# Kernel tuning notes

Measured on AMD Instinct MI355X. Metric: run time of the kernel, lower is better.

The kernel has to match this reference:

```python
import jax, jax.numpy as jnp
import numpy as np

B, S, H, E, A = 64, 1024, 1024, 1024, 1024

def setup_inputs() -> dict:
    key = jax.random.key(0)
    k1, k2, k3, k4, k5 = jax.random.split(key, 5)
    return {
        "decoder_state": jax.random.normal(k1, (B, H), dtype=jnp.float32),
        "encoder_outputs": jax.random.normal(k2, (B, S, E), dtype=jnp.float32),
        "src_mask": jnp.ones((B, S), dtype=bool),
        "W_a": jax.random.normal(k3, (H, A), dtype=jnp.float32) / np.sqrt(H),
        "U_a": jax.random.normal(k4, (E, A), dtype=jnp.float32) / np.sqrt(E),
        "v_a": jax.random.normal(k5, (A,), dtype=jnp.float32) / np.sqrt(A),
    }

def reference(decoder_state, encoder_outputs, src_mask, W_a, U_a, v_a):
    # k_dec: [B, 1, A], k_enc: [B, S, A]
    k_dec = jnp.einsum('bh,ha->ba', decoder_state, W_a)[:, None, :]
    k_enc = jnp.einsum('bse,ea->bsa', encoder_outputs, U_a)
    att_hidden = jnp.tanh(k_dec + k_enc)
    scores = jnp.einsum('bsa,a->bs', att_hidden, v_a)
    scores = scores + (~src_mask).astype(scores.dtype) * (-1e9)
    weights = jax.nn.softmax(scores, axis=-1)
    ctx = jnp.einsum('bs,bse->be', weights, encoder_outputs)
    return (ctx, weights)
```

## Files before the change

kernel.cpp:

```cpp
#include <hip/hip_runtime.h>
#include <hip/hip_bf16.h>
#include <math.h>

#define NB 64
#define NS 1024
#define NH 1024
#define NE 1024
#define NA 1024

#define BM 128
#define BN 128
#define BK 64

typedef __attribute__((ext_vector_type(8))) short bf16x8;
typedef __attribute__((ext_vector_type(4))) float f32x4;

__device__ __forceinline__ unsigned short f2bf(float x) {
    __hip_bfloat16 h = __float2bfloat16(x);
    return *reinterpret_cast<unsigned short*>(&h);
}
__device__ __forceinline__ float bf2f(unsigned short u) {
    __hip_bfloat16 h = *reinterpret_cast<__hip_bfloat16*>(&u);
    return __bfloat162float(h);
}
__device__ __forceinline__ float tanh_fast(float x) {
    float ax = fabsf(x);
    float e = __expf(-2.f * ax);
    float r = (1.f - e) / (1.f + e);
    return x < 0.f ? -r : r;
}
__device__ __forceinline__ int swz(int row, int colBf16) {
    return (row * 128 + colBf16 * 2) ^ ((row & 7) << 4);
}

__global__ __launch_bounds__(256) void split_uat_kernel(
    const float* __restrict__ Ua,
    unsigned short* __restrict__ uatHi, unsigned short* __restrict__ uatLo)
{
    __shared__ float tile[32][33];
    const int e0 = blockIdx.x * 32, a0 = blockIdx.y * 32;
    const int tx = threadIdx.x & 31, ty = threadIdx.x >> 5;
#pragma unroll
    for (int j = 0; j < 4; ++j)
        tile[ty + j * 8][tx] = Ua[(size_t)(e0 + ty + j * 8) * NA + a0 + tx];
    __syncthreads();
#pragma unroll
    for (int j = 0; j < 4; ++j) {
        const int a = a0 + ty + j * 8;
        const float x = tile[tx][ty + j * 8];
        const unsigned short h = f2bf(x);
        const unsigned short l = f2bf(x - bf2f(h));
        uatHi[(size_t)a * NE + e0 + tx] = h;
        uatLo[(size_t)a * NE + e0 + tx] = l;
    }
}

__global__ __launch_bounds__(256) void kdec_kernel(
    const float* __restrict__ dec, const float* __restrict__ Wa,
    float* __restrict__ kdec)
{
    __shared__ float dls[NH];
    const int b = blockIdx.x;
    const int a = blockIdx.y * 256 + threadIdx.x;
    for (int i = threadIdx.x; i < NH; i += 256) dls[i] = dec[b * NH + i];
    __syncthreads();
    float acc = 0.f;
#pragma unroll 8
    for (int h = 0; h < NH; ++h) acc += dls[h] * Wa[(size_t)h * NA + a];
    kdec[b * NA + a] = acc;
}

__global__ __launch_bounds__(256, 2) void scores_kernel(
    const float* __restrict__ enc,
    const unsigned short* __restrict__ uatHi, const unsigned short* __restrict__ uatLo,
    const float* __restrict__ kdec, const float* __restrict__ va,
    float* __restrict__ scores)
{
    __shared__ __align__(16) char aHi[BM * BK * 2];
    __shared__ __align__(16) char aLo[BM * BK * 2];
    __shared__ __align__(16) char bHi[BN * BK * 2];
    __shared__ __align__(16) char bLo[BN * BK * 2];
    __shared__ float scLds[2][BM];

    const int t    = threadIdx.x;
    const int b    = blockIdx.y;
    const int s0   = blockIdx.x * BM;
    const int lane = t & 63;
    const int wid  = t >> 6;
    const int wr   = wid >> 1;
    const int wc   = wid & 1;
    const int lr   = lane & 15;
    const int lk   = (lane >> 4) * 8;

    const float* encB = enc + ((size_t)b * NS + s0) * NE;

    float scp[4][4];
#pragma unroll
    for (int i = 0; i < 4; ++i)
#pragma unroll
        for (int r = 0; r < 4; ++r) scp[i][r] = 0.f;

    for (int ac = 0; ac < NA / BN; ++ac) {
        const int a0 = ac * BN;
        f32x4 acc[4][4];
#pragma unroll
        for (int fi = 0; fi < 4; ++fi)
#pragma unroll
            for (int fj = 0; fj < 4; ++fj) acc[fi][fj] = (f32x4){0.f, 0.f, 0.f, 0.f};

        for (int e0 = 0; e0 < NE; e0 += BK) {
            __syncthreads();
#pragma unroll
            for (int it = 0; it < 8; ++it) {
                const int flat = t + it * 256;
                const int row  = flat >> 4;
                const int c4   = (flat & 15) * 4;
                const float4 v = *reinterpret_cast<const float4*>(
                    encB + (size_t)row * NE + e0 + c4);
                ushort4 h, l;
                h.x = f2bf(v.x); l.x = f2bf(v.x - bf2f(h.x));
                h.y = f2bf(v.y); l.y = f2bf(v.y - bf2f(h.y));
                h.z = f2bf(v.z); l.z = f2bf(v.z - bf2f(h.z));
                h.w = f2bf(v.w); l.w = f2bf(v.w - bf2f(h.w));
                *reinterpret_cast<ushort4*>(aHi + swz(row, c4)) = h;
                *reinterpret_cast<ushort4*>(aLo + swz(row, c4)) = l;
            }
#pragma unroll
            for (int it = 0; it < 4; ++it) {
                const int flat = t + it * 256;
                const int row  = flat >> 3;
                const int c8   = (flat & 7) * 8;
                const size_t g = (size_t)(a0 + row) * NE + e0 + c8;
                *reinterpret_cast<int4*>(bHi + swz(row, c8)) =
                    *reinterpret_cast<const int4*>(uatHi + g);
                *reinterpret_cast<int4*>(bLo + swz(row, c8)) =
                    *reinterpret_cast<const int4*>(uatLo + g);
            }
            __syncthreads();

#pragma unroll
            for (int ks = 0; ks < BK; ks += 32) {
                bf16x8 aH[4], aL[4], bH[4], bL[4];
#pragma unroll
                for (int f = 0; f < 4; ++f) {
                    aH[f] = *reinterpret_cast<const bf16x8*>(aHi + swz(wr * 64 + f * 16 + lr, ks + lk));
                    aL[f] = *reinterpret_cast<const bf16x8*>(aLo + swz(wr * 64 + f * 16 + lr, ks + lk));
                    bH[f] = *reinterpret_cast<const bf16x8*>(bHi + swz(wc * 64 + f * 16 + lr, ks + lk));
                    bL[f] = *reinterpret_cast<const bf16x8*>(bLo + swz(wc * 64 + f * 16 + lr, ks + lk));
                }
#pragma unroll
                for (int fi = 0; fi < 4; ++fi)
#pragma unroll
                    for (int fj = 0; fj < 4; ++fj) {
                        acc[fi][fj] = __builtin_amdgcn_mfma_f32_16x16x32_bf16(aH[fi], bH[fj], acc[fi][fj], 0, 0, 0);
                        acc[fi][fj] = __builtin_amdgcn_mfma_f32_16x16x32_bf16(aH[fi], bL[fj], acc[fi][fj], 0, 0, 0);
                        acc[fi][fj] = __builtin_amdgcn_mfma_f32_16x16x32_bf16(aL[fi], bH[fj], acc[fi][fj], 0, 0, 0);
                    }
            }
        }

#pragma unroll
        for (int fj = 0; fj < 4; ++fj) {
            const int a = a0 + wc * 64 + fj * 16 + lr;
            const float kd = kdec[(size_t)b * NA + a];
            const float vv = va[a];
#pragma unroll
            for (int fi = 0; fi < 4; ++fi)
#pragma unroll
                for (int r = 0; r < 4; ++r)
                    scp[fi][r] += tanh_fast(kd + acc[fi][fj][r]) * vv;
        }
    }

#pragma unroll
    for (int fi = 0; fi < 4; ++fi)
#pragma unroll
        for (int r = 0; r < 4; ++r) {
            float v = scp[fi][r];
            v += __shfl_xor(v, 1);
            v += __shfl_xor(v, 2);
            v += __shfl_xor(v, 4);
            v += __shfl_xor(v, 8);
            if (lr == 0)
                scLds[wc][wr * 64 + fi * 16 + (lane >> 4) * 4 + r] = v;
        }
    __syncthreads();
    if (t < BM)
        scores[(size_t)b * NS + s0 + t] = scLds[0][t] + scLds[1][t];
}

__global__ __launch_bounds__(256) void softmax_kernel(
    const float* __restrict__ scores, const int* __restrict__ mask,
    float* __restrict__ out )
{
    __shared__ float red[8];
    const int b = blockIdx.x;
    const int t = threadIdx.x;
    float v[4];
    float mx = -INFINITY;
#pragma unroll
    for (int i = 0; i < 4; ++i) {
        const int s = t + i * 256;
        float x = scores[b * NS + s];
        if (mask[b * NS + s] == 0) x += -1e9f;
        v[i] = x;
        mx = fmaxf(mx, x);
    }
    for (int off = 1; off < 64; off <<= 1) mx = fmaxf(mx, __shfl_xor(mx, off));
    const int wid = t >> 6;
    if ((t & 63) == 0) red[wid] = mx;
    __syncthreads();
    mx = fmaxf(fmaxf(red[0], red[1]), fmaxf(red[2], red[3]));
    float sum = 0.f;
#pragma unroll
    for (int i = 0; i < 4; ++i) { v[i] = expf(v[i] - mx); sum += v[i]; }
    for (int off = 1; off < 64; off <<= 1) sum += __shfl_xor(sum, off);
    if ((t & 63) == 0) red[4 + wid] = sum;
    __syncthreads();
    sum = red[4] + red[5] + red[6] + red[7];
    const float inv = 1.f / sum;
#pragma unroll
    for (int i = 0; i < 4; ++i) {
        const int s = t + i * 256;
        out[NB * NE + b * NS + s] = v[i] * inv;
        out[b * NE + s] = 0.f;
    }
}

__global__ __launch_bounds__(256) void ctx_kernel(
    const float* __restrict__ enc, const float* __restrict__ w,
    float* __restrict__ ctx)
{
    __shared__ float wls[128];
    const int b  = blockIdx.x;
    const int ec = blockIdx.y;
    const int ss = blockIdx.z;
    const int t  = threadIdx.x;
    if (t < 128) wls[t] = w[b * NS + ss * 128 + t];
    __syncthreads();
    const int e = ec * 256 + t;
    const float* p = enc + ((size_t)b * NS + ss * 128) * NE + e;
    float acc = 0.f;
#pragma unroll 4
    for (int s = 0; s < 128; ++s) acc += wls[s] * p[(size_t)s * NE];
    atomicAdd(&ctx[b * NE + e], acc);
}

extern "C" void kernel_launch(void* const* d_in, const int* in_sizes, int n_in,
                              void* d_out, int out_size, void* d_ws, size_t ws_size,
                              hipStream_t stream)
{
    const float* dec  = (const float*)d_in[0];
    const float* enc  = (const float*)d_in[1];
    const int*   mask = (const int*)d_in[2];
    const float* Wa   = (const float*)d_in[3];
    const float* Ua   = (const float*)d_in[4];
    const float* va   = (const float*)d_in[5];
    float* out = (float*)d_out;

    float* kdec            = (float*)d_ws;
    float* scores          = kdec + NB * NA;
    unsigned short* uatHi  = (unsigned short*)(scores + NB * NS);
    unsigned short* uatLo  = uatHi + (size_t)NA * NE;

    split_uat_kernel<<<dim3(NE / 32, NA / 32), 256, 0, stream>>>(Ua, uatHi, uatLo);
    kdec_kernel<<<dim3(NB, NA / 256), 256, 0, stream>>>(dec, Wa, kdec);
    scores_kernel<<<dim3(NS / BM, NB), 256, 0, stream>>>(enc, uatHi, uatLo, kdec, va, scores);
    softmax_kernel<<<dim3(NB), 256, 0, stream>>>(scores, mask, out);
    ctx_kernel<<<dim3(NB, NE / 256, NS / 128), 256, 0, stream>>>(enc, out + NB * NE, out);
}
```

Baseline: 1.369 ms.

## Pre-split encoder into swizzled bf16 tiles and stream via direct-to-LDS loads

Adds kernels that pre-split the encoder outputs and U_a into hi/lo bf16 halves laid out as swizzled 128x64 tiles in workspace. A new 512-thread scores kernel double-buffers these tiles into LDS with global_load_lds and issues the MFMA work against them, so the fp32-to-bf16 split is no longer redone inside the GEMM loop for every A-chunk. This costs an extra 256MB workspace write and read for the encoder copy and a separate pass over it, and the new path only runs when the workspace is large enough; otherwise it falls back to the old path.

```diff
diff --git a/kernel.cpp b/kernel.cpp
--- a/kernel.cpp
+++ b/kernel.cpp
@@ -11,6 +11,8 @@
 #define BM 128
 #define BN 128
 #define BK 64
+#define TILE_BYTES 16384
+#define TILE_ELEMS 8192
 
 typedef __attribute__((ext_vector_type(8))) short bf16x8;
 typedef __attribute__((ext_vector_type(4))) float f32x4;
@@ -32,6 +34,203 @@
 __device__ __forceinline__ int swz(int row, int colBf16) {
     return (row * 128 + colBf16 * 2) ^ ((row & 7) << 4);
 }
+__device__ __forceinline__ void gload_lds16(const void* g, void* l) {
+    __builtin_amdgcn_global_load_lds(
+        (const __attribute__((address_space(1))) unsigned int*)g,
+        (__attribute__((address_space(3))) unsigned int*)l, 16, 0, 0);
+}
+
+
+__global__ __launch_bounds__(256) void split_enc_kernel(
+    const float* __restrict__ enc,
+    unsigned short* __restrict__ encHiT, unsigned short* __restrict__ encLoT)
+{
+    const int sblk = blockIdx.x;
+    const int b    = blockIdx.y;
+    const int t    = threadIdx.x;
+    const float* src = enc + ((size_t)b * NS + sblk * 128) * NE;
+    char* hiB = (char*)encHiT + (size_t)(b * 8 + sblk) * 16 * TILE_BYTES;
+    char* loB = (char*)encLoT + (size_t)(b * 8 + sblk) * 16 * TILE_BYTES;
+    for (int eblk = 0; eblk < 16; ++eblk) {
+        char* hiT = hiB + (size_t)eblk * TILE_BYTES;
+        char* loT = loB + (size_t)eblk * TILE_BYTES;
+#pragma unroll
+        for (int j = 0; j < 8; ++j) {
+            const int flat = t + j * 256;
+            const int row  = flat >> 4;
+            const int c4   = (flat & 15) * 4;
+            const float4 v = *reinterpret_cast<const float4*>(
+                src + (size_t)row * NE + eblk * 64 + c4);
+            ushort4 h, l;
+            h.x = f2bf(v.x); l.x = f2bf(v.x - bf2f(h.x));
+            h.y = f2bf(v.y); l.y = f2bf(v.y - bf2f(h.y));
+            h.z = f2bf(v.z); l.z = f2bf(v.z - bf2f(h.z));
+            h.w = f2bf(v.w); l.w = f2bf(v.w - bf2f(h.w));
+            *reinterpret_cast<ushort4*>(hiT + swz(row, c4)) = h;
+            *reinterpret_cast<ushort4*>(loT + swz(row, c4)) = l;
+        }
+    }
+}
+
+__global__ __launch_bounds__(256) void split_uat_tiled_kernel(
+    const float* __restrict__ Ua,
+    unsigned short* __restrict__ uatHiT, unsigned short* __restrict__ uatLoT)
+{
+    __shared__ float ls[64][132];
+    const int ablk = blockIdx.x;
+    const int eblk = blockIdx.y;
+    const int t = threadIdx.x;
+    const int a0 = ablk * 128, e0 = eblk * 64;
+#pragma unroll
+    for (int j = 0; j < 8; ++j) {
+        const int flat = t + j * 256;
+        const int e  = flat >> 5;
+        const int c4 = (flat & 31) * 4;
+        *reinterpret_cast<float4*>(&ls[e][c4]) =
+            *reinterpret_cast<const float4*>(Ua + (size_t)(e0 + e) * NA + a0 + c4);
+    }
+    __syncthreads();
+    char* hiT = (char*)uatHiT + (size_t)(ablk * 16 + eblk) * TILE_BYTES;
+    char* loT = (char*)uatLoT + (size_t)(ablk * 16 + eblk) * TILE_BYTES;
+#pragma unroll
+    for (int j = 0; j < 8; ++j) {
+        const int flat = t + j * 256;
+        const int a  = flat >> 4;
+        const int e4 = (flat & 15) * 4;
+        const float x0 = ls[e4 + 0][a], x1 = ls[e4 + 1][a];
+        const float x2 = ls[e4 + 2][a], x3 = ls[e4 + 3][a];
+        ushort4 h, l;
+        h.x = f2bf(x0); l.x = f2bf(x0 - bf2f(h.x));
+        h.y = f2bf(x1); l.y = f2bf(x1 - bf2f(h.y));
+        h.z = f2bf(x2); l.z = f2bf(x2 - bf2f(h.z));
+        h.w = f2bf(x3); l.w = f2bf(x3 - bf2f(h.w));
+        *reinterpret_cast<ushort4*>(hiT + swz(a, e4)) = h;
+        *reinterpret_cast<ushort4*>(loT + swz(a, e4)) = l;
+    }
+}
+
+__global__ __launch_bounds__(512, 1) void scores_mfma_kernel(
+    const unsigned short* __restrict__ encHiT, const unsigned short* __restrict__ encLoT,
+    const unsigned short* __restrict__ uatHiT, const unsigned short* __restrict__ uatLoT,
+    const float* __restrict__ kdec, const float* __restrict__ va,
+    float* __restrict__ scores)
+{
+    __shared__ __align__(16) char lds[2][65536];
+    __shared__ float scLds[4][BM];
+
+    const int t    = threadIdx.x;
+    const int sblk = blockIdx.x;
+    const int b    = blockIdx.y;
+    const int lane = t & 63;
+    const int wid  = t >> 6;
+    const int wr   = wid >> 2;
+    const int wc   = wid & 3;
+    const int lr   = lane & 15;
+    const int lk   = (lane >> 4) * 8;
+
+    const char* aHiB = (const char*)encHiT + (size_t)(b * 8 + sblk) * 16 * TILE_BYTES;
+    const char* aLoB = (const char*)encLoT + (size_t)(b * 8 + sblk) * 16 * TILE_BYTES;
+    const char* bHiB = (const char*)uatHiT;
+    const char* bLoB = (const char*)uatLoT;
+
+    auto STAGE = [&](int buf, int g) {
+        const int ac = g >> 4, eblk = g & 15;
+        const char* aHi = aHiB + (size_t)eblk * TILE_BYTES;
+        const char* aLo = aLoB + (size_t)eblk * TILE_BYTES;
+        const char* bHi = bHiB + (size_t)(ac * 16 + eblk) * TILE_BYTES;
+        const char* bLo = bLoB + (size_t)(ac * 16 + eblk) * TILE_BYTES;
+        char* dst = &lds[buf][0];
+#pragma unroll
+        for (int j = 0; j < 8; ++j) {
+            const char* sb = (j < 2) ? aHi : (j < 4) ? aLo : (j < 6) ? bHi : bLo;
+            const char* src = sb + ((j & 1) * 512 + t) * 16;
+            char* dstp = dst + (j * 512 + wid * 64) * 16;
+            gload_lds16(src, dstp);
+        }
+    };
+
+    float scp[4][4];
+#pragma unroll
+    for (int i = 0; i < 4; ++i)
+#pragma unroll
+        for (int r = 0; r < 4; ++r) scp[i][r] = 0.f;
+
+    STAGE(0, 0);
+    __syncthreads();
+
+    int cur = 0;
+    for (int ac = 0; ac < 8; ++ac) {
+        f32x4 acc[4][2];
+#pragma unroll
+        for (int fi = 0; fi < 4; ++fi)
+#pragma unroll
+            for (int fj = 0; fj < 2; ++fj) acc[fi][fj] = (f32x4){0.f, 0.f, 0.f, 0.f};
+
+        for (int e0i = 0; e0i < 16; ++e0i) {
+            const int g = ac * 16 + e0i;
+            if (g + 1 < 128) STAGE(cur ^ 1, g + 1);
+
+            const char* L = &lds[cur][0];
+#pragma unroll
+            for (int ks = 0; ks < 2; ++ks) {
+                const int col = ks * 32 + lk;
+                bf16x8 aH[4], aL[4], bH[2], bL[2];
+#pragma unroll
+                for (int f = 0; f < 4; ++f) {
+                    const int so = swz(wr * 64 + f * 16 + lr, col);
+                    aH[f] = *reinterpret_cast<const bf16x8*>(L + so);
+                    aL[f] = *reinterpret_cast<const bf16x8*>(L + 16384 + so);
+                }
+#pragma unroll
+                for (int f = 0; f < 2; ++f) {
+                    const int so = swz(wc * 32 + f * 16 + lr, col);
+                    bH[f] = *reinterpret_cast<const bf16x8*>(L + 32768 + so);
+                    bL[f] = *reinterpret_cast<const bf16x8*>(L + 49152 + so);
+                }
+#pragma unroll
+                for (int fi = 0; fi < 4; ++fi)
+#pragma unroll
+                    for (int fj = 0; fj < 2; ++fj) {
+                        acc[fi][fj] = __builtin_amdgcn_mfma_f32_16x16x32_bf16(aH[fi], bH[fj], acc[fi][fj], 0, 0, 0);
+                        acc[fi][fj] = __builtin_amdgcn_mfma_f32_16x16x32_bf16(aH[fi], bL[fj], acc[fi][fj], 0, 0, 0);
+                        acc[fi][fj] = __builtin_amdgcn_mfma_f32_16x16x32_bf16(aL[fi], bH[fj], acc[fi][fj], 0, 0, 0);
+                    }
+            }
+            __syncthreads();
+            cur ^= 1;
+        }
+
+#pragma unroll
+        for (int fj = 0; fj < 2; ++fj) {
+            const int a = ac * BN + wc * 32 + fj * 16 + lr;
+            const float kd = kdec[(size_t)b * NA + a];
+            const float vv = va[a];
+#pragma unroll
+            for (int fi = 0; fi < 4; ++fi)
+#pragma unroll
+                for (int r = 0; r < 4; ++r)
+                    scp[fi][r] += tanh_fast(kd + acc[fi][fj][r]) * vv;
+        }
+    }
+
+#pragma unroll
+    for (int fi = 0; fi < 4; ++fi)
+#pragma unroll
+        for (int r = 0; r < 4; ++r) {
+            float v = scp[fi][r];
+            v += __shfl_xor(v, 1);
+            v += __shfl_xor(v, 2);
+            v += __shfl_xor(v, 4);
+            v += __shfl_xor(v, 8);
+            if (lr == 0)
+                scLds[wc][wr * 64 + fi * 16 + (lane >> 4) * 4 + r] = v;
+        }
+    __syncthreads();
+    if (t < BM)
+        scores[(size_t)b * NS + sblk * BM + t] =
+            scLds[0][t] + scLds[1][t] + scLds[2][t] + scLds[3][t];
+}
+
 
 __global__ __launch_bounds__(256) void split_uat_kernel(
     const float* __restrict__ Ua,
@@ -53,21 +252,6 @@
         uatHi[(size_t)a * NE + e0 + tx] = h;
         uatLo[(size_t)a * NE + e0 + tx] = l;
     }
-}
-
-__global__ __launch_bounds__(256) void kdec_kernel(
-    const float* __restrict__ dec, const float* __restrict__ Wa,
-    float* __restrict__ kdec)
-{
-    __shared__ float dls[NH];
-    const int b = blockIdx.x;
-    const int a = blockIdx.y * 256 + threadIdx.x;
-    for (int i = threadIdx.x; i < NH; i += 256) dls[i] = dec[b * NH + i];
-    __syncthreads();
-    float acc = 0.f;
-#pragma unroll 8
-    for (int h = 0; h < NH; ++h) acc += dls[h] * Wa[(size_t)h * NA + a];
-    kdec[b * NA + a] = acc;
 }
 
 __global__ __launch_bounds__(256, 2) void scores_kernel(
@@ -112,9 +296,9 @@
             __syncthreads();
 #pragma unroll
             for (int it = 0; it < 8; ++it) {
-                const int flat = t + it * 256;
-                const int row  = flat >> 4;
-                const int c4   = (flat & 15) * 4;
+                int flat = t + it * 256;
+                int row  = flat >> 4;
+                int c4   = (flat & 15) * 4;
                 const float4 v = *reinterpret_cast<const float4*>(
                     encB + (size_t)row * NE + e0 + c4);
                 ushort4 h, l;
@@ -127,9 +311,9 @@
             }
 #pragma unroll
             for (int it = 0; it < 4; ++it) {
-                const int flat = t + it * 256;
-                const int row  = flat >> 3;
-                const int c8   = (flat & 7) * 8;
+                int flat = t + it * 256;
+                int row  = flat >> 3;
+                int c8   = (flat & 7) * 8;
                 const size_t g = (size_t)(a0 + row) * NE + e0 + c8;
                 *reinterpret_cast<int4*>(bHi + swz(row, c8)) =
                     *reinterpret_cast<const int4*>(uatHi + g);
@@ -158,7 +342,6 @@
                     }
             }
         }
-
 #pragma unroll
         for (int fj = 0; fj < 4; ++fj) {
             const int a = a0 + wc * 64 + fj * 16 + lr;
@@ -171,7 +354,6 @@
                     scp[fi][r] += tanh_fast(kd + acc[fi][fj][r]) * vv;
         }
     }
-
 #pragma unroll
     for (int fi = 0; fi < 4; ++fi)
 #pragma unroll
@@ -189,9 +371,25 @@
         scores[(size_t)b * NS + s0 + t] = scLds[0][t] + scLds[1][t];
 }
 
+
+__global__ __launch_bounds__(256) void kdec_kernel(
+    const float* __restrict__ dec, const float* __restrict__ Wa,
+    float* __restrict__ kdec)
+{
+    __shared__ float dls[NH];
+    const int b = blockIdx.x;
+    const int a = blockIdx.y * 256 + threadIdx.x;
+    for (int i = threadIdx.x; i < NH; i += 256) dls[i] = dec[b * NH + i];
+    __syncthreads();
+    float acc = 0.f;
+#pragma unroll 8
+    for (int h = 0; h < NH; ++h) acc += dls[h] * Wa[(size_t)h * NA + a];
+    kdec[b * NA + a] = acc;
+}
+
 __global__ __launch_bounds__(256) void softmax_kernel(
     const float* __restrict__ scores, const int* __restrict__ mask,
-    float* __restrict__ out )
+    float* __restrict__ out)
 {
     __shared__ float red[8];
     const int b = blockIdx.x;
@@ -258,14 +456,32 @@
     const float* va   = (const float*)d_in[5];
     float* out = (float*)d_out;
 
-    float* kdec            = (float*)d_ws;
-    float* scores          = kdec + NB * NA;
-    unsigned short* uatHi  = (unsigned short*)(scores + NB * NS);
-    unsigned short* uatLo  = uatHi + (size_t)NA * NE;
-
-    split_uat_kernel<<<dim3(NE / 32, NA / 32), 256, 0, stream>>>(Ua, uatHi, uatLo);
+    float* kdec   = (float*)d_ws;
+    float* scores = kdec + NB * NA;
+    unsigned short* w0 = (unsigned short*)(scores + NB * NS);
+
+    const size_t uatElems = (size_t)NA * NE;
+    const size_t encElems = (size_t)NB * NS * NE;
+    const size_t needA = 512ull * 1024 + 2 * uatElems * 2 + 2 * encElems * 2;
+
     kdec_kernel<<<dim3(NB, NA / 256), 256, 0, stream>>>(dec, Wa, kdec);
-    scores_kernel<<<dim3(NS / BM, NB), 256, 0, stream>>>(enc, uatHi, uatLo, kdec, va, scores);
+
+    if (ws_size >= needA) {
+        unsigned short* uatHiT = w0;
+        unsigned short* uatLoT = uatHiT + uatElems;
+        unsigned short* encHiT = uatLoT + uatElems;
+        unsigned short* encLoT = encHiT + encElems;
+        split_uat_tiled_kernel<<<dim3(8, 16), 256, 0, stream>>>(Ua, uatHiT, uatLoT);
+        split_enc_kernel<<<dim3(8, NB), 256, 0, stream>>>(enc, encHiT, encLoT);
+        scores_mfma_kernel<<<dim3(8, NB), 512, 0, stream>>>(
+            encHiT, encLoT, uatHiT, uatLoT, kdec, va, scores);
+    } else {
+        unsigned short* uatHi = w0;
+        unsigned short* uatLo = uatHi + uatElems;
+        split_uat_kernel<<<dim3(NE / 32, NA / 32), 256, 0, stream>>>(Ua, uatHi, uatLo);
+        scores_kernel<<<dim3(NS / BM, NB), 256, 0, stream>>>(enc, uatHi, uatLo, kdec, va, scores);
+    }
+
     softmax_kernel<<<dim3(NB), 256, 0, stream>>>(scores, mask, out);
     ctx_kernel<<<dim3(NB, NE / 256, NS / 128), 256, 0, stream>>>(enc, out + NB * NE, out);
 }
```

New measurement: 1.123 ms. 1.22x faster.

## Pre-split encoder to bf16 tiles and triple-buffer scores GEMM via direct LDS loads

Applied to the files above, without the earlier changes.

Adds a kernel that splits the encoder outputs into hi/lo bf16 halves in a pre-swizzled tiled layout. U_a is retiled the same way. The scores GEMM becomes a 512-thread, 128x256 tile kernel that streams these tiles into a 3-stage LDS ring with global_load_lds and explicit waitcnt/barriers, and raises wave priority around the MFMA block. This removes the in-loop fp32-to-bf16 conversion and register-staged loads from the GEMM and overlaps memory with compute. The cost is an extra full pass that writes 256MB of split encoder data to the workspace and reads it back.

```diff
diff --git a/kernel.cpp b/kernel.cpp
--- a/kernel.cpp
+++ b/kernel.cpp
@@ -8,11 +8,13 @@
 #define NE 1024
 #define NA 1024
 
-#define BM 128
-#define BN 128
-#define BK 64
+#define A_TILE 8192
+#define B_TILE 16384
+#define BUF_BYTES 49152
+#define NT 128
 
 typedef __attribute__((ext_vector_type(8))) short bf16x8;
+typedef __attribute__((ext_vector_type(8))) unsigned short ushort8_t;
 typedef __attribute__((ext_vector_type(4))) float f32x4;
 
 __device__ __forceinline__ unsigned short f2bf(float x) {
@@ -29,29 +31,74 @@
     float r = (1.f - e) / (1.f + e);
     return x < 0.f ? -r : r;
 }
-__device__ __forceinline__ int swz(int row, int colBf16) {
-    return (row * 128 + colBf16 * 2) ^ ((row & 7) << 4);
+__device__ __forceinline__ int swz32(int row, int bcol) {
+    return row * 64 + (bcol ^ (((row >> 1) & 3) << 4));
+}
+__device__ __forceinline__ void gload_lds16(const void* g, void* l) {
+    __builtin_amdgcn_global_load_lds(
+        (const __attribute__((address_space(1))) unsigned int*)g,
+        (__attribute__((address_space(3))) unsigned int*)l, 16, 0, 0);
+}
+
+__global__ __launch_bounds__(256) void split_enc_kernel(
+    const float* __restrict__ enc,
+    unsigned short* __restrict__ encHiT, unsigned short* __restrict__ encLoT)
+{
+    const int sblk = blockIdx.x;
+    const int b    = blockIdx.y;
+    const int t    = threadIdx.x;
+    const float* src = enc + ((size_t)b * NS + sblk * 128) * NE;
+    char* hiB = (char*)encHiT + (size_t)(b * 8 + sblk) * 32 * A_TILE;
+    char* loB = (char*)encLoT + (size_t)(b * 8 + sblk) * 32 * A_TILE;
+    const int et   = t >> 3;
+    const int bcol = (t & 7) * 8;
+    for (int row = 0; row < 128; ++row) {
+        const float4 v = *reinterpret_cast<const float4*>(src + (size_t)row * NE + t * 4);
+        ushort4 h, l;
+        h.x = f2bf(v.x); l.x = f2bf(v.x - bf2f(h.x));
+        h.y = f2bf(v.y); l.y = f2bf(v.y - bf2f(h.y));
+        h.z = f2bf(v.z); l.z = f2bf(v.z - bf2f(h.z));
+        h.w = f2bf(v.w); l.w = f2bf(v.w - bf2f(h.w));
+        const int off = (size_t)et * A_TILE + swz32(row, bcol);
+        *reinterpret_cast<ushort4*>(hiB + off) = h;
+        *reinterpret_cast<ushort4*>(loB + off) = l;
+    }
 }
 
 __global__ __launch_bounds__(256) void split_uat_kernel(
     const float* __restrict__ Ua,
-    unsigned short* __restrict__ uatHi, unsigned short* __restrict__ uatLo)
-{
-    __shared__ float tile[32][33];
-    const int e0 = blockIdx.x * 32, a0 = blockIdx.y * 32;
-    const int tx = threadIdx.x & 31, ty = threadIdx.x >> 5;
-#pragma unroll
-    for (int j = 0; j < 4; ++j)
-        tile[ty + j * 8][tx] = Ua[(size_t)(e0 + ty + j * 8) * NA + a0 + tx];
-    __syncthreads();
-#pragma unroll
-    for (int j = 0; j < 4; ++j) {
-        const int a = a0 + ty + j * 8;
-        const float x = tile[tx][ty + j * 8];
-        const unsigned short h = f2bf(x);
-        const unsigned short l = f2bf(x - bf2f(h));
-        uatHi[(size_t)a * NE + e0 + tx] = h;
-        uatLo[(size_t)a * NE + e0 + tx] = l;
+    unsigned short* __restrict__ uatHiT, unsigned short* __restrict__ uatLoT)
+{
+    __shared__ float ls[32][257];
+    const int ac = blockIdx.x;
+    const int eb = blockIdx.y;
+    const int t  = threadIdx.x;
+    const int a0 = ac * 256, e0 = eb * 32;
+#pragma unroll
+    for (int p = 0; p < 8; ++p) {
+        const int flat = p * 256 + t;
+        const int e = flat >> 6, q = flat & 63;
+        *reinterpret_cast<float4*>(&ls[e][q * 4]) =
+            *reinterpret_cast<const float4*>(Ua + (size_t)(e0 + e) * NA + a0 + q * 4);
+    }
+    __syncthreads();
+    char* hiT = (char*)uatHiT + (size_t)(ac * 32 + eb) * B_TILE;
+    char* loT = (char*)uatLoT + (size_t)(ac * 32 + eb) * B_TILE;
+#pragma unroll
+    for (int p = 0; p < 4; ++p) {
+        const int flat = p * 256 + t;
+        const int a = flat >> 2, o = flat & 3;
+        ushort8_t h8, l8;
+#pragma unroll
+        for (int j = 0; j < 8; ++j) {
+            const float x = ls[o * 8 + j][a];
+            const unsigned short hh = f2bf(x);
+            h8[j] = hh;
+            l8[j] = f2bf(x - bf2f(hh));
+        }
+        const int off = swz32(a, o * 16);
+        *reinterpret_cast<int4*>(hiT + off) = *reinterpret_cast<int4*>(&h8);
+        *reinterpret_cast<int4*>(loT + off) = *reinterpret_cast<int4*>(&l8);
     }
 }
 
@@ -70,29 +117,63 @@
     kdec[b * NA + a] = acc;
 }
 
-__global__ __launch_bounds__(256, 2) void scores_kernel(
-    const float* __restrict__ enc,
-    const unsigned short* __restrict__ uatHi, const unsigned short* __restrict__ uatLo,
+__global__ __launch_bounds__(512, 2) void scores_mfma2_kernel(
+    const unsigned short* __restrict__ encHiT, const unsigned short* __restrict__ encLoT,
+    const unsigned short* __restrict__ uatHiT, const unsigned short* __restrict__ uatLoT,
     const float* __restrict__ kdec, const float* __restrict__ va,
     float* __restrict__ scores)
 {
-    __shared__ __align__(16) char aHi[BM * BK * 2];
-    __shared__ __align__(16) char aLo[BM * BK * 2];
-    __shared__ __align__(16) char bHi[BN * BK * 2];
-    __shared__ __align__(16) char bLo[BN * BK * 2];
-    __shared__ float scLds[2][BM];
+    __shared__ __align__(16) char lds[3 * BUF_BYTES];
+    __shared__ float scLds[4][128];
 
     const int t    = threadIdx.x;
+    const int sblk = blockIdx.x;
     const int b    = blockIdx.y;
-    const int s0   = blockIdx.x * BM;
     const int lane = t & 63;
     const int wid  = t >> 6;
-    const int wr   = wid >> 1;
-    const int wc   = wid & 1;
-    const int lr   = lane & 15;
-    const int lk   = (lane >> 4) * 8;
-
-    const float* encB = enc + ((size_t)b * NS + s0) * NE;
+    const int wr   = wid >> 2;
+    const int wc   = wid & 3;
+    const int lrow = lane & 15;
+    const int kb   = (lane >> 4) * 16;
+
+    const char* aHiB = (const char*)encHiT + (size_t)(b * 8 + sblk) * 32 * A_TILE;
+    const char* aLoB = (const char*)encLoT + (size_t)(b * 8 + sblk) * 32 * A_TILE;
+    const char* bHiB = (const char*)uatHiT;
+    const char* bLoB = (const char*)uatLoT;
+
+    int aOff[4], bOff[4];
+#pragma unroll
+    for (int f = 0; f < 4; ++f) {
+        aOff[f] = swz32(wr * 64 + f * 16 + lrow, kb);
+        bOff[f] = swz32(wc * 64 + f * 16 + lrow, kb);
+    }
+
+    float kd[4][4], vv[4][4];
+#pragma unroll
+    for (int ac = 0; ac < 4; ++ac)
+#pragma unroll
+        for (int fj = 0; fj < 4; ++fj) {
+            const int a = ac * 256 + wc * 64 + fj * 16 + lrow;
+            kd[ac][fj] = kdec[(size_t)b * NA + a];
+            vv[ac][fj] = va[a];
+        }
+
+    auto STAGE = [&](int g, int buf) {
+        const int ac2 = g >> 5, et2 = g & 31;
+        const char* aHi = aHiB + (size_t)et2 * A_TILE;
+        const char* aLo = aLoB + (size_t)et2 * A_TILE;
+        const char* bHi = bHiB + (size_t)(ac2 * 32 + et2) * B_TILE;
+        const char* bLo = bLoB + (size_t)(ac2 * 32 + et2) * B_TILE;
+        char* dst = lds + buf * BUF_BYTES;
+        const int so = t * 16;
+        const int wo = wid * 1024;
+        gload_lds16(aHi + so,        dst + 0 * 8192 + wo);
+        gload_lds16(aLo + so,        dst + 1 * 8192 + wo);
+        gload_lds16(bHi + so,        dst + 2 * 8192 + wo);
+        gload_lds16(bHi + 8192 + so, dst + 3 * 8192 + wo);
+        gload_lds16(bLo + so,        dst + 4 * 8192 + wo);
+        gload_lds16(bLo + 8192 + so, dst + 5 * 8192 + wo);
+    };
 
     float scp[4][4];
 #pragma unroll
@@ -100,76 +181,63 @@
 #pragma unroll
         for (int r = 0; r < 4; ++r) scp[i][r] = 0.f;
 
-    for (int ac = 0; ac < NA / BN; ++ac) {
-        const int a0 = ac * BN;
+    STAGE(0, 0);
+    STAGE(1, 1);
+
+    int cur = 0;
+#pragma unroll
+    for (int ac = 0; ac < 4; ++ac) {
         f32x4 acc[4][4];
 #pragma unroll
         for (int fi = 0; fi < 4; ++fi)
 #pragma unroll
             for (int fj = 0; fj < 4; ++fj) acc[fi][fj] = (f32x4){0.f, 0.f, 0.f, 0.f};
 
-        for (int e0 = 0; e0 < NE; e0 += BK) {
-            __syncthreads();
-#pragma unroll
-            for (int it = 0; it < 8; ++it) {
-                const int flat = t + it * 256;
-                const int row  = flat >> 4;
-                const int c4   = (flat & 15) * 4;
-                const float4 v = *reinterpret_cast<const float4*>(
-                    encB + (size_t)row * NE + e0 + c4);
-                ushort4 h, l;
-                h.x = f2bf(v.x); l.x = f2bf(v.x - bf2f(h.x));
-                h.y = f2bf(v.y); l.y = f2bf(v.y - bf2f(h.y));
-                h.z = f2bf(v.z); l.z = f2bf(v.z - bf2f(h.z));
-                h.w = f2bf(v.w); l.w = f2bf(v.w - bf2f(h.w));
-                *reinterpret_cast<ushort4*>(aHi + swz(row, c4)) = h;
-                *reinterpret_cast<ushort4*>(aLo + swz(row, c4)) = l;
+        for (int et = 0; et < 32; ++et) {
+            const int g = ac * 32 + et;
+            if (g + 2 < NT) {
+                int nb = cur + 2; if (nb >= 3) nb -= 3;
+                STAGE(g + 2, nb);
+                asm volatile("s_waitcnt vmcnt(12)" ::: "memory");
+            } else if (g + 1 < NT) {
+                asm volatile("s_waitcnt vmcnt(6)" ::: "memory");
+            } else {
+                asm volatile("s_waitcnt vmcnt(0)" ::: "memory");
             }
-#pragma unroll
-            for (int it = 0; it < 4; ++it) {
-                const int flat = t + it * 256;
-                const int row  = flat >> 3;
-                const int c8   = (flat & 7) * 8;
-                const size_t g = (size_t)(a0 + row) * NE + e0 + c8;
-                *reinterpret_cast<int4*>(bHi + swz(row, c8)) =
-                    *reinterpret_cast<const int4*>(uatHi + g);
-                *reinterpret_cast<int4*>(bLo + swz(row, c8)) =
-                    *reinterpret_cast<const int4*>(uatLo + g);
+            asm volatile("s_barrier" ::: "memory");
+
+            const char* L = lds + cur * BUF_BYTES;
+            bf16x8 aH[4], aL[4], bH[4], bL[4];
+#pragma unroll
+            for (int f = 0; f < 4; ++f) {
+                aH[f] = *reinterpret_cast<const bf16x8*>(L + aOff[f]);
+                aL[f] = *reinterpret_cast<const bf16x8*>(L + A_TILE + aOff[f]);
+                bH[f] = *reinterpret_cast<const bf16x8*>(L + 2 * A_TILE + bOff[f]);
+                bL[f] = *reinterpret_cast<const bf16x8*>(L + 2 * A_TILE + B_TILE + bOff[f]);
             }
-            __syncthreads();
-
-#pragma unroll
-            for (int ks = 0; ks < BK; ks += 32) {
-                bf16x8 aH[4], aL[4], bH[4], bL[4];
-#pragma unroll
-                for (int f = 0; f < 4; ++f) {
-                    aH[f] = *reinterpret_cast<const bf16x8*>(aHi + swz(wr * 64 + f * 16 + lr, ks + lk));
-                    aL[f] = *reinterpret_cast<const bf16x8*>(aLo + swz(wr * 64 + f * 16 + lr, ks + lk));
-                    bH[f] = *reinterpret_cast<const bf16x8*>(bHi + swz(wc * 64 + f * 16 + lr, ks + lk));
-                    bL[f] = *reinterpret_cast<const bf16x8*>(bLo + swz(wc * 64 + f * 16 + lr, ks + lk));
+            __builtin_amdgcn_s_setprio(1);
+#pragma unroll
+            for (int fi = 0; fi < 4; ++fi)
+#pragma unroll
+                for (int fj = 0; fj < 4; ++fj) {
+                    acc[fi][fj] = __builtin_amdgcn_mfma_f32_16x16x32_bf16(aH[fi], bH[fj], acc[fi][fj], 0, 0, 0);
+                    acc[fi][fj] = __builtin_amdgcn_mfma_f32_16x16x32_bf16(aH[fi], bL[fj], acc[fi][fj], 0, 0, 0);
+                    acc[fi][fj] = __builtin_amdgcn_mfma_f32_16x16x32_bf16(aL[fi], bH[fj], acc[fi][fj], 0, 0, 0);
                 }
-#pragma unroll
-                for (int fi = 0; fi < 4; ++fi)
-#pragma unroll
-                    for (int fj = 0; fj < 4; ++fj) {
-                        acc[fi][fj] = __builtin_amdgcn_mfma_f32_16x16x32_bf16(aH[fi], bH[fj], acc[fi][fj], 0, 0, 0);
-                        acc[fi][fj] = __builtin_amdgcn_mfma_f32_16x16x32_bf16(aH[fi], bL[fj], acc[fi][fj], 0, 0, 0);
-                        acc[fi][fj] = __builtin_amdgcn_mfma_f32_16x16x32_bf16(aL[fi], bH[fj], acc[fi][fj], 0, 0, 0);
-                    }
-            }
+            __builtin_amdgcn_s_setprio(0);
+            __builtin_amdgcn_sched_barrier(0);
+            asm volatile("s_waitcnt lgkmcnt(0)" ::: "memory");
+            asm volatile("s_barrier" ::: "memory");
+            cur += 1; if (cur >= 3) cur -= 3;
         }
 
 #pragma unroll
-        for (int fj = 0; fj < 4; ++fj) {
-            const int a = a0 + wc * 64 + fj * 16 + lr;
-            const float kd = kdec[(size_t)b * NA + a];
-            const float vv = va[a];
+        for (int fj = 0; fj < 4; ++fj)
 #pragma unroll
             for (int fi = 0; fi < 4; ++fi)
 #pragma unroll
                 for (int r = 0; r < 4; ++r)
-                    scp[fi][r] += tanh_fast(kd + acc[fi][fj][r]) * vv;
-        }
+                    scp[fi][r] += tanh_fast(kd[ac][fj] + acc[fi][fj][r]) * vv[ac][fj];
     }
 
 #pragma unroll
@@ -181,17 +249,18 @@
             v += __shfl_xor(v, 2);
             v += __shfl_xor(v, 4);
             v += __shfl_xor(v, 8);
-            if (lr == 0)
+            if (lrow == 0)
                 scLds[wc][wr * 64 + fi * 16 + (lane >> 4) * 4 + r] = v;
         }
     __syncthreads();
-    if (t < BM)
-        scores[(size_t)b * NS + s0 + t] = scLds[0][t] + scLds[1][t];
+    if (t < 128)
+        scores[(size_t)b * NS + sblk * 128 + t] =
+            scLds[0][t] + scLds[1][t] + scLds[2][t] + scLds[3][t];
 }
 
 __global__ __launch_bounds__(256) void softmax_kernel(
     const float* __restrict__ scores, const int* __restrict__ mask,
-    float* __restrict__ out )
+    float* __restrict__ out)
 {
     __shared__ float red[8];
     const int b = blockIdx.x;
@@ -258,14 +327,18 @@
     const float* va   = (const float*)d_in[5];
     float* out = (float*)d_out;
 
-    float* kdec            = (float*)d_ws;
-    float* scores          = kdec + NB * NA;
-    unsigned short* uatHi  = (unsigned short*)(scores + NB * NS);
-    unsigned short* uatLo  = uatHi + (size_t)NA * NE;
-
-    split_uat_kernel<<<dim3(NE / 32, NA / 32), 256, 0, stream>>>(Ua, uatHi, uatLo);
+    float* kdec   = (float*)d_ws;
+    float* scores = kdec + NB * NA;
+    unsigned short* uatHiT = (unsigned short*)(scores + NB * NS);
+    unsigned short* uatLoT = uatHiT + (size_t)NA * NE;
+    unsigned short* encHiT = uatLoT + (size_t)NA * NE;
+    unsigned short* encLoT = encHiT + (size_t)NB * NS * NE;
+
     kdec_kernel<<<dim3(NB, NA / 256), 256, 0, stream>>>(dec, Wa, kdec);
-    scores_kernel<<<dim3(NS / BM, NB), 256, 0, stream>>>(enc, uatHi, uatLo, kdec, va, scores);
+    split_uat_kernel<<<dim3(4, 32), 256, 0, stream>>>(Ua, uatHiT, uatLoT);
+    split_enc_kernel<<<dim3(8, NB), 256, 0, stream>>>(enc, encHiT, encLoT);
+    scores_mfma2_kernel<<<dim3(8, NB), 512, 0, stream>>>(
+        encHiT, encLoT, uatHiT, uatLoT, kdec, va, scores);
     softmax_kernel<<<dim3(NB), 256, 0, stream>>>(scores, mask, out);
     ctx_kernel<<<dim3(NB, NE / 256, NS / 128), 256, 0, stream>>>(enc, out + NB * NE, out);
 }
```

Result: faster. 1.097 ms (-19.8%).
